# Performance work log

Hardware: AMD Instinct MI355X
Metric: run time of the kernel (lower is better)

## Reference

```python
import jax, jax.numpy as jnp
import numpy as np

B, S, H = 2, 4096, 1024
NKH, NVH, DK, DV = 8, 16, 64, 64
KEY_DIM = NKH * DK
VAL_DIM = NVH * DV
CONV_DIM = 2 * KEY_DIM + VAL_DIM
KSZ = 4
EPS = 1e-6


def setup_inputs() -> dict:
    key = jax.random.key(0)
    ks = jax.random.split(key, 8)
    s = 0.02
    return {
        "hidden_states": jax.random.normal(ks[0], (B, S, H), jnp.float32),
        "W_qkv": jax.random.normal(ks[1], (CONV_DIM, H), jnp.float32) * s,
        "conv_w": jax.random.normal(ks[2], (CONV_DIM, 1, KSZ), jnp.float32) * 0.1,
        "W_z": jax.random.normal(ks[3], (VAL_DIM, H), jnp.float32) * s,
        "W_b": jax.random.normal(ks[4], (NVH, H), jnp.float32) * s,
        "W_a": jax.random.normal(ks[5], (NVH, H), jnp.float32) * s,
        "dt_bias": jnp.ones((NVH,), jnp.float32),
        "A_log": jnp.log(jax.random.uniform(ks[6], (NVH,), jnp.float32, 0.1, 16.0)),
        "norm_weight": jnp.ones((DV,), jnp.float32),
        "W_out": jax.random.normal(ks[7], (H, VAL_DIM), jnp.float32) * s,
    }


def _forward(hidden_states, W_qkv, conv_w, W_z, W_b, W_a, dt_bias, A_log, norm_weight, W_out):
    b, s, _ = hidden_states.shape
    # fused qkv projection -> depthwise causal conv -> silu
    mixed = hidden_states @ W_qkv.T                       # [b,s,conv_dim]
    x = mixed.transpose(0, 2, 1)                          # [b,conv_dim,s]
    y = jax.lax.conv_general_dilated(
        x, conv_w, (1,), [(KSZ - 1, 0)],
        dimension_numbers=("NCH", "OIH", "NCH"),
        feature_group_count=CONV_DIM)                     # causal: left pad k-1
    mixed = jax.nn.silu(y).transpose(0, 2, 1)             # [b,s,conv_dim]

    z = (hidden_states @ W_z.T).reshape(b, s, NVH, DV)
    beta = jax.nn.sigmoid(hidden_states @ W_b.T)          # [b,s,nvh]
    a = hidden_states @ W_a.T
    g = -jnp.exp(A_log) * jax.nn.softplus(a + dt_bias)    # [b,s,nvh]

    q, k, v = jnp.split(mixed, [KEY_DIM, 2 * KEY_DIM], axis=-1)
    q = q.reshape(b, s, NKH, DK)
    k = k.reshape(b, s, NKH, DK)
    v = v.reshape(b, s, NVH, DV)
    rep = NVH // NKH
    if rep > 1:  # GQA: repeat_interleave along head dim
        q = jnp.repeat(q, rep, axis=2)
        k = jnp.repeat(k, rep, axis=2)
    q = q * (DK ** -0.5)

    # gated delta-rule recurrence over time (state: [b,h,dk,dv])
    def step(Sst, inp):
        q_t, k_t, v_t, g_t, b_t = inp                     # [b,h,dk],[b,h,dk],[b,h,dv],[b,h],[b,h]
        Sst = Sst * jnp.exp(g_t)[..., None, None]
        kv = jnp.einsum("bhkv,bhk->bhv", Sst, k_t)
        delta = (v_t - kv) * b_t[..., None]
        Sst = Sst + k_t[..., None] * delta[..., None, :]
        o = jnp.einsum("bhkv,bhk->bhv", Sst, q_t)
        return Sst, o

    S0 = jnp.zeros((b, NVH, DK, DV), jnp.float32)
    xs = (q.transpose(1, 0, 2, 3), k.transpose(1, 0, 2, 3), v.transpose(1, 0, 2, 3),
          g.transpose(1, 0, 2), beta.transpose(1, 0, 2))
    _, o = jax.lax.scan(step, S0, xs)                     # o: [s,b,h,dv]
    o = o.transpose(1, 0, 2, 3)                           # [b,s,h,dv]

    # gated RMSNorm over head_v_dim: x * silu(z), rmsnorm, * weight
    h_ = o * jax.nn.silu(z)
    var = jnp.mean(h_ * h_, axis=-1, keepdims=True)
    h_ = h_ * jax.lax.rsqrt(var + EPS) * norm_weight

    return h_.reshape(b, s, VAL_DIM) @ W_out.T            # [b,s,hidden]


def reference(hidden_states, W_qkv, conv_w, W_z, W_b, W_a, dt_bias, A_log, norm_weight, W_out):
    return _forward(hidden_states, W_qkv, conv_w, W_z, W_b, W_a, dt_bias, A_log, norm_weight, W_out)
```

## Files before the change

kernel.cpp:

```cpp
#include <hip/hip_runtime.h>
#include <hip/hip_bf16.h>
#include <stdint.h>

#define B_    2
#define S_    4096
#define H_    1024
#define NKH_  8
#define NVH_  16
#define DK_   64
#define DV_   64
#define KEYD_ 512
#define CDIM_ 2048
#define VALD_ 1024
#define NCHUNK_ 64
#define CS_   64

using bf16 = __hip_bfloat16;
using bf16x8 = __attribute__((ext_vector_type(8))) short;
using f32x4  = __attribute__((ext_vector_type(4))) float;

__device__ inline float bsh2f(short s) {
  union { ushort u; bf16 h; } c; c.u = (ushort)s; return __bfloat162float(c.h);
}
__device__ inline short f2bsh(float f) {
  union { ushort u; bf16 h; } c; c.h = __float2bfloat16(f); return (short)c.u;
}

__device__ __forceinline__ void gload16(const bf16* g, short* lds) {
  __builtin_amdgcn_global_load_lds(
      (const __attribute__((address_space(1))) void*)g,
      (__attribute__((address_space(3))) void*)lds, 16, 0, 0);
}

__global__ __launch_bounds__(256) void castf2b(const float* __restrict__ x,
                                               bf16* __restrict__ y, long n) {
  const long i = ((long)blockIdx.x * 256 + threadIdx.x) * 4;
  if (i >= n) return;
  float4 v = *(const float4*)(x + i);
  union { ushort4 u; bf16 h[4]; } o;
  o.h[0] = __float2bfloat16(v.x);
  o.h[1] = __float2bfloat16(v.y);
  o.h[2] = __float2bfloat16(v.z);
  o.h[3] = __float2bfloat16(v.w);
  *(ushort4*)(y + i) = o.u;
}

template <typename OT>
__global__ __launch_bounds__(256) void gemm_bt(const bf16* __restrict__ A,
                                               const bf16* __restrict__ Bm,
                                               OT* __restrict__ C,
                                               int M, int N, int K) {
  __shared__ short Asm[128 * 32];
  __shared__ short Bsm[128 * 32];
  const int t = threadIdx.x;
  const int w = t >> 6, l = t & 63;
  const int ntn = N >> 7;
  const int bm = blockIdx.x / ntn, bn = blockIdx.x % ntn;
  const int m0 = bm << 7, n0 = bn << 7;
  const int wm = (w >> 1) << 6, wn = (w & 1) << 6;

  f32x4 acc[4][4] = {};

  const int grow = l >> 2;
  const int gc8 = (l & 3) << 3;
  const bf16* Agl = A + (long)m0 * K + gc8;
  const bf16* Bgl = Bm + (long)n0 * K + gc8;

  const int lm = l & 15;
  const int kk = (l >> 4) << 3;
  const short* ar0 = &Asm[(wm + lm) * 32 + kk];
  const short* br0 = &Bsm[(wn + lm) * 32 + kk];

  for (int k0 = 0; k0 < K; k0 += 32) {
    __syncthreads();
#pragma unroll
    for (int j = 0; j < 2; ++j) {
      const int s = w * 2 + j;
      gload16(Agl + (long)(s * 16 + grow) * K + k0, &Asm[s * 16 * 32]);
      gload16(Bgl + (long)(s * 16 + grow) * K + k0, &Bsm[s * 16 * 32]);
    }
    __syncthreads();
    bf16x8 af[4], bfr[4];
#pragma unroll
    for (int mi = 0; mi < 4; ++mi) af[mi] = *(const bf16x8*)(ar0 + mi * 16 * 32);
#pragma unroll
    for (int ni = 0; ni < 4; ++ni) bfr[ni] = *(const bf16x8*)(br0 + ni * 16 * 32);
#pragma unroll
    for (int mi = 0; mi < 4; ++mi)
#pragma unroll
      for (int ni = 0; ni < 4; ++ni)
        acc[mi][ni] = __builtin_amdgcn_mfma_f32_16x16x32_bf16(af[mi], bfr[ni],
                                                              acc[mi][ni], 0, 0, 0);
  }

  const int r0 = (l >> 4) << 2;
  const int cn = l & 15;
#pragma unroll
  for (int mi = 0; mi < 4; ++mi)
#pragma unroll
    for (int ni = 0; ni < 4; ++ni) {
      long base = (long)(m0 + wm + mi * 16 + r0) * N + (n0 + wn + ni * 16 + cn);
#pragma unroll
      for (int r = 0; r < 4; ++r) {
        if constexpr (sizeof(OT) == 2)
          C[base + (long)r * N] = __float2bfloat16(acc[mi][ni][r]);
        else
          C[base + (long)r * N] = acc[mi][ni][r];
      }
    }
}

__global__ __launch_bounds__(256) void conv3(const bf16* __restrict__ mixed,
                                             const float* __restrict__ cw,
                                             bf16* __restrict__ qkv) {
  const long idx = (long)blockIdx.x * 256 + threadIdx.x;
  const int c0 = (int)(idx & 255) << 3;
  const long row = idx >> 8;
  const int s = (int)(row & (S_ - 1));

  bf16x8 mv[4];
#pragma unroll
  for (int j = 0; j < 4; ++j) {
    if (s - 3 + j >= 0)
      mv[j] = *(const bf16x8*)(mixed + (row + j - 3) * CDIM_ + c0);
    else
      mv[j] = (bf16x8){0, 0, 0, 0, 0, 0, 0, 0};
  }

  const float qs = (c0 < KEYD_) ? 0.125f : 1.f;
  union { ushort4 u4[2]; short h[8]; } o;
#pragma unroll
  for (int e = 0; e < 8; ++e) {
    const float4 w = *(const float4*)(cw + (c0 + e) * 4);
    float acc = 0.f;
    acc = fmaf(w.x, bsh2f(mv[0][e]), acc);
    acc = fmaf(w.y, bsh2f(mv[1][e]), acc);
    acc = fmaf(w.z, bsh2f(mv[2][e]), acc);
    acc = fmaf(w.w, bsh2f(mv[3][e]), acc);
    const float y = qs * (acc / (1.f + __expf(-acc)));
    o.h[e] = f2bsh(y);
  }
  *(bf16x8*)((uint16_t*)qkv + row * CDIM_ + c0) = *(bf16x8*)&o.h[0];
}

__global__ __launch_bounds__(256) void proj_ba2(const float* __restrict__ hs,
                                                const float* __restrict__ Wb,
                                                const float* __restrict__ Wa,
                                                const float* __restrict__ dtb,
                                                const float* __restrict__ Alog,
                                                float* __restrict__ beta,
                                                float* __restrict__ g) {
  __shared__ float4 hrow[8][257];
  const long row0 = (long)blockIdx.x * 8;
  const int tid = threadIdx.x;
  for (int i = tid; i < 2048; i += 256) {
    const int r = i >> 8, c4 = i & 255;
    hrow[r][c4] = *(const float4*)(hs + (row0 + r) * H_ + (long)c4 * 4);
  }
  __syncthreads();
  const int j = tid >> 3, r = tid & 7;
  const float4* Wp = (const float4*)(j < 16 ? Wb + (long)j * H_
                                            : Wa + (long)(j - 16) * H_);
  float4 a4 = {0.f, 0.f, 0.f, 0.f};
#pragma unroll 4
  for (int i = 0; i < 256; ++i) {
    const float4 w = Wp[i];
    const float4 hv = hrow[r][i];
    a4.x = fmaf(w.x, hv.x, a4.x);
    a4.y = fmaf(w.y, hv.y, a4.y);
    a4.z = fmaf(w.z, hv.z, a4.z);
    a4.w = fmaf(w.w, hv.w, a4.w);
  }
  const float acc = (a4.x + a4.y) + (a4.z + a4.w);
  const long row = row0 + r;
  if (j < 16) {
    beta[row * NVH_ + j] = 1.f / (1.f + __expf(-acc));
  } else {
    const int hh = j - 16;
    const float x = acc + dtb[hh];
    const float sp = (x > 20.f) ? x : log1pf(__expf(x));
    g[row * NVH_ + hh] = -__expf(Alog[hh]) * sp;
  }
}

__global__ __launch_bounds__(256) void chunk_pre(const bf16* __restrict__ qkv,
                                                 const float* __restrict__ beta,
                                                 const float* __restrict__ g,
                                                 bf16* __restrict__ Wws,
                                                 bf16* __restrict__ U0ws,
                                                 float* __restrict__ lgws,
                                                 bf16* __restrict__ McT,
                                                 bf16* __restrict__ Bc) {
  __shared__ short Ksm[64][72];
  __shared__ short Vsm[64][72];
  __shared__ float Tsm[64][64];
  __shared__ short KpT[64][72];
  __shared__ float Xl[128][67];
  __shared__ float lgs[64];
  __shared__ float bts[64];
  __shared__ float belg[64];

  short (*XB)[36]   = (short (*)[36]) & Vsm[0][0];
  short (*TloB)[40] = (short (*)[40]) & Ksm[0][0];
  short (*WT)[72]   = (short (*)[72]) & Tsm[0][0];
  short (*U0T)[72]  = Vsm;

  const int blk = blockIdx.x;
  const int hb = blk & 31, c = blk >> 5;
  const long task = (long)hb * 64 + c;
  const int h = hb & 15, b = hb >> 4, kh = h >> 1;
  const long t0 = (long)b * S_ + (long)c * CS_;
  const int tid = threadIdx.x;
  const int wv = tid >> 6, l = tid & 63;
  const int lm = l & 15, lk8 = (l >> 4) << 3;
  const int r0 = (l >> 4) << 2, cn = l & 15;
  const int srow = tid >> 2, scol = (tid & 3) * 16;

  {
    const bf16* kp = qkv + (t0 + srow) * CDIM_ + KEYD_ + kh * 64 + scol;
    const bf16* vp = qkv + (t0 + srow) * CDIM_ + 2 * KEYD_ + h * 64 + scol;
    *(bf16x8*)&Ksm[srow][scol]     = *(const bf16x8*)(kp);
    *(bf16x8*)&Ksm[srow][scol + 8] = *(const bf16x8*)(kp + 8);
    *(bf16x8*)&Vsm[srow][scol]     = *(const bf16x8*)(vp);
    *(bf16x8*)&Vsm[srow][scol + 8] = *(const bf16x8*)(vp + 8);
  }
  if (tid < 64) {
    bts[tid] = beta[(t0 + tid) * NVH_ + h];
    lgs[tid] = g[(t0 + tid) * NVH_ + h];
  }
  __syncthreads();

  if (tid < 64) {
    float x = lgs[tid];
#pragma unroll
    for (int d = 1; d < 64; d <<= 1) {
      const float y = __shfl_up(x, d);
      if (tid >= d) x += y;
    }
    lgs[tid] = x;
    belg[tid] = bts[tid] * __expf(x);
  }
  __syncthreads();

  if (tid < 128) {
    f32x4 acc[2][4] = {};
#pragma unroll
    for (int ks = 0; ks < 2; ++ks) {
      bf16x8 bfr[4];
#pragma unroll
      for (int ni = 0; ni < 4; ++ni)
        bfr[ni] = *(const bf16x8*)&Ksm[ni * 16 + lm][lk8 + ks * 32];
#pragma unroll
      for (int mi = 0; mi < 2; ++mi) {
        bf16x8 afr = *(const bf16x8*)&Ksm[(wv * 2 + mi) * 16 + lm][lk8 + ks * 32];
#pragma unroll
        for (int ni = 0; ni < 4; ++ni)
          acc[mi][ni] = __builtin_amdgcn_mfma_f32_16x16x32_bf16(afr, bfr[ni],
                                                                acc[mi][ni], 0, 0, 0);
      }
    }
#pragma unroll
    for (int mi = 0; mi < 2; ++mi)
#pragma unroll
      for (int ni = 0; ni < 4; ++ni)
#pragma unroll
        for (int r = 0; r < 4; ++r) {
          const int t = (wv * 2 + mi) * 16 + r0 + r;
          const int i = ni * 16 + cn;
          Tsm[t][i] = (i < t) ? bts[t] * __expf(lgs[t] - lgs[i]) * acc[mi][ni][r]
                              : 0.f;
        }
  } else {
    const int idx = tid - 128;
    const int tt = idx >> 1;
    const int o2 = (idx & 1) * 32;
    const float dec = __expf(lgs[63] - lgs[tt]);
#pragma unroll 8
    for (int k = 0; k < 32; ++k)
      KpT[o2 + k][tt] = f2bsh(dec * bsh2f(Ksm[tt][o2 + k]));
  }
  __syncthreads();

  auto solve32 = [&](int base) {
    for (int j = base; j < base + 32; j += 8) {
      float xs[8];
#pragma unroll
      for (int a = 0; a < 8; ++a) xs[a] = Xl[tid][j + a];
#pragma unroll
      for (int a = 1; a < 8; ++a)
#pragma unroll
        for (int bb = 0; bb < a; ++bb)
          xs[a] = fmaf(-Tsm[j + a][j + bb], xs[bb], xs[a]);
#pragma unroll
      for (int a = 1; a < 8; ++a) Xl[tid][j + a] = xs[a];
      const int tend = base + 32;
#pragma unroll 2
      for (int tt = j + 8; tt < tend; ++tt) {
        const float4 ta = *(const float4*)&Tsm[tt][j];
        const float4 tb = *(const float4*)&Tsm[tt][j + 4];
        float v = Xl[tid][tt];
        v = fmaf(-ta.x, xs[0], v); v = fmaf(-ta.y, xs[1], v);
        v = fmaf(-ta.z, xs[2], v); v = fmaf(-ta.w, xs[3], v);
        v = fmaf(-tb.x, xs[4], v); v = fmaf(-tb.y, xs[5], v);
        v = fmaf(-tb.z, xs[6], v); v = fmaf(-tb.w, xs[7], v);
        Xl[tid][tt] = v;
      }
    }
  };

  if (tid < 128) {
    const int colW = tid & 63;
    const bool isW = tid < 64;
#pragma unroll 8
    for (int t = 0; t < CS_; ++t)
      Xl[tid][t] = isW ? belg[t] * bsh2f(Ksm[t][colW])
                       : bts[t] * bsh2f(Vsm[t][colW]);
    solve32(0);
  }
  if (tid < 64) lgws[task * 64 + tid] = lgs[tid];
  __syncthreads();

  {
    const int col = tid & 127, uh = (tid >> 7) * 16;
#pragma unroll
    for (int u = 0; u < 16; ++u)
      XB[col][uh + u] = f2bsh(Xl[col][uh + u]);
  }
  if (tid < 128) {
    const int m = tid >> 2, u0 = (tid & 3) * 8;
#pragma unroll
    for (int u = 0; u < 8; ++u)
      TloB[m][u0 + u] = f2bsh(Tsm[32 + m][u0 + u]);
  }
  __syncthreads();

  {
#pragma unroll
    for (int ni2 = 0; ni2 < 2; ++ni2) {
      const int ni = wv * 2 + ni2;
      bf16x8 bfr = *(const bf16x8*)&XB[ni * 16 + lm][lk8];
#pragma unroll
      for (int mi = 0; mi < 2; ++mi) {
        bf16x8 afr = *(const bf16x8*)&TloB[mi * 16 + lm][lk8];
        f32x4 uacc = {};
        uacc = __builtin_amdgcn_mfma_f32_16x16x32_bf16(afr, bfr, uacc, 0, 0, 0);
#pragma unroll
        for (int r = 0; r < 4; ++r)
          Xl[ni * 16 + cn][32 + mi * 16 + r0 + r] -= uacc[r];
      }
    }
  }
  __syncthreads();

  if (tid < 128) solve32(32);
  __syncthreads();

  if (tid < 128) {
    const int colW = tid & 63;
    const bool isW = tid < 64;
    bf16* dst = (isW ? Wws : U0ws) + task * 4096 + colW;
    short (*XT)[72] = isW ? WT : U0T;
#pragma unroll 4
    for (int t = 0; t < CS_; t += 2) {
      const float v0 = Xl[tid][t], v1 = Xl[tid][t + 1];
      dst[(long)t * 64] = __float2bfloat16(v0);
      dst[(long)(t + 1) * 64] = __float2bfloat16(v1);
      short2 pk; pk.x = f2bsh(v0); pk.y = f2bsh(v1);
      *(short2*)&XT[colW][t] = pk;
    }
  }
  __syncthreads();

  {
    f32x4 macc[4] = {};
#pragma unroll
    for (int ks = 0; ks < 2; ++ks) {
      bf16x8 afr = *(const bf16x8*)&KpT[wv * 16 + lm][lk8 + ks * 32];
#pragma unroll
      for (int ni = 0; ni < 4; ++ni) {
        bf16x8 bfr = *(const bf16x8*)&WT[ni * 16 + lm][lk8 + ks * 32];
        macc[ni] = __builtin_amdgcn_mfma_f32_16x16x32_bf16(afr, bfr, macc[ni], 0, 0, 0);
      }
    }
#pragma unroll
    for (int ni = 0; ni < 4; ++ni)
#pragma unroll
      for (int r = 0; r < 4; ++r)
        McT[task * 4096 + (wv * 16 + r0 + r) * 64 + ni * 16 + cn] =
            __float2bfloat16(-macc[ni][r]);
  }
  {
    f32x4 bacc[4] = {};
#pragma unroll
    for (int ks = 0; ks < 2; ++ks) {
      bf16x8 afr = *(const bf16x8*)&U0T[wv * 16 + lm][lk8 + ks * 32];
#pragma unroll
      for (int ni = 0; ni < 4; ++ni) {
        bf16x8 bfr = *(const bf16x8*)&KpT[ni * 16 + lm][lk8 + ks * 32];
        bacc[ni] = __builtin_amdgcn_mfma_f32_16x16x32_bf16(afr, bfr, bacc[ni], 0, 0, 0);
      }
    }
#pragma unroll
    for (int ni = 0; ni < 4; ++ni)
#pragma unroll
      for (int r = 0; r < 4; ++r)
        Bc[task * 4096 + (wv * 16 + r0 + r) * 64 + ni * 16 + cn] =
            __float2bfloat16(bacc[ni][r]);
  }
}

__global__ __launch_bounds__(256) void chunk_state(const bf16* __restrict__ McT,
                                                   const bf16* __restrict__ Bc,
                                                   const float* __restrict__ lgws,
                                                   bf16* __restrict__ Sb) {
  __shared__ short Msm[3][64][72];
  __shared__ short Bsm[3][64][72];
  __shared__ short Ssm[64][72];
  __shared__ float lgb[3];

  const int hb = blockIdx.x;
  const int tid = threadIdx.x, wv = tid >> 6, l = tid & 63;
  const int lm = l & 15, lk8 = (l >> 4) << 3;
  const int r0 = (l >> 4) << 2, cn = l & 15;
  const int srow = tid >> 2, scol = (tid & 3) * 16;

  for (int i = tid; i < 64 * 72; i += 256) ((short*)Ssm)[i] = 0;
  f32x4 Sreg[4] = {};

  auto stage = [&](int cc, int bu) {
    const long tt = (long)hb * 64 + cc;
    const bf16* mp = McT + tt * 4096 + srow * 64 + scol;
    const bf16* bp = Bc + tt * 4096 + srow * 64 + scol;
    *(bf16x8*)&Msm[bu][srow][scol]     = *(const bf16x8*)(mp);
    *(bf16x8*)&Msm[bu][srow][scol + 8] = *(const bf16x8*)(mp + 8);
    *(bf16x8*)&Bsm[bu][srow][scol]     = *(const bf16x8*)(bp);
    *(bf16x8*)&Bsm[bu][srow][scol + 8] = *(const bf16x8*)(bp + 8);
    if (tid == 0) lgb[bu] = lgws[tt * 64 + 63];
  };
  stage(0, 0);
  stage(1, 1);

  for (int c = 0; c < NCHUNK_; ++c) {
    __syncthreads();
    if (c + 2 < NCHUNK_) stage(c + 2, (c + 2) % 3);
    const int bu = c % 3;

    {
      bf16* sp = Sb + ((long)hb * 64 + c) * 4096;
#pragma unroll
      for (int ni = 0; ni < 4; ++ni)
#pragma unroll
        for (int r = 0; r < 4; ++r)
          sp[(wv * 16 + r0 + r) * 64 + ni * 16 + cn] = __float2bfloat16(Sreg[ni][r]);
    }

    bf16x8 sfr0 = *(const bf16x8*)&Ssm[wv * 16 + lm][lk8];
    bf16x8 sfr1 = *(const bf16x8*)&Ssm[wv * 16 + lm][lk8 + 32];
    f32x4 kacc[4] = {};
#pragma unroll
    for (int ni = 0; ni < 4; ++ni) {
      bf16x8 b0 = *(const bf16x8*)&Msm[bu][ni * 16 + lm][lk8];
      kacc[ni] = __builtin_amdgcn_mfma_f32_16x16x32_bf16(sfr0, b0, kacc[ni], 0, 0, 0);
      bf16x8 b1 = *(const bf16x8*)&Msm[bu][ni * 16 + lm][lk8 + 32];
      kacc[ni] = __builtin_amdgcn_mfma_f32_16x16x32_bf16(sfr1, b1, kacc[ni], 0, 0, 0);
    }
    const float eend = __expf(lgb[bu]);
#pragma unroll
    for (int ni = 0; ni < 4; ++ni)
#pragma unroll
      for (int r = 0; r < 4; ++r) {
        const float bv = bsh2f(Bsm[bu][wv * 16 + r0 + r][ni * 16 + cn]);
        Sreg[ni][r] = eend * Sreg[ni][r] + kacc[ni][r] + bv;
        Ssm[wv * 16 + r0 + r][ni * 16 + cn] = f2bsh(Sreg[ni][r]);
      }
  }
}

__global__ __launch_bounds__(256) void chunk_out(const bf16* __restrict__ qkv,
                                                 const bf16* __restrict__ Wws,
                                                 const bf16* __restrict__ U0ws,
                                                 const float* __restrict__ lgws,
                                                 const bf16* __restrict__ Sb,
                                                 float* __restrict__ o) {
  __shared__ short Qsm[64][72];
  __shared__ short Ksm[64][72];
  __shared__ short Wsm[64][72];
  __shared__ short Usm[64][72];
  __shared__ short Amm[64][72];
  __shared__ short Dsm[64][72];
  __shared__ float lgs[64];

  const int blk = blockIdx.x;
  const int hb = blk & 31, c = blk >> 5;
  const long task = (long)hb * 64 + c;
  const int h = hb & 15, b = hb >> 4, kh = h >> 1;
  const long sb = (long)b * S_ + (long)c * CS_;
  const int tid = threadIdx.x, wv = tid >> 6, l = tid & 63;
  const int lm = l & 15, lk8 = (l >> 4) << 3;
  const int r0 = (l >> 4) << 2, cn = l & 15;
  const int srow = tid >> 2, scol = (tid & 3) * 16;

  const bf16* sp = Sb + task * 4096 + (wv * 16 + lm) * 64 + lk8;
  bf16x8 sfr0 = *(const bf16x8*)(sp);
  bf16x8 sfr1 = *(const bf16x8*)(sp + 32);

  {
    const bf16* qp = qkv + (sb + srow) * CDIM_ + kh * 64 + scol;
    const bf16* kp = qkv + (sb + srow) * CDIM_ + KEYD_ + kh * 64 + scol;
    const bf16* wp = Wws + task * 4096 + srow * 64 + scol;
    const bf16* up = U0ws + task * 4096 + srow * 64 + scol;
    *(bf16x8*)&Qsm[srow][scol]     = *(const bf16x8*)(qp);
    *(bf16x8*)&Qsm[srow][scol + 8] = *(const bf16x8*)(qp + 8);
    *(bf16x8*)&Ksm[srow][scol]     = *(const bf16x8*)(kp);
    *(bf16x8*)&Ksm[srow][scol + 8] = *(const bf16x8*)(kp + 8);
    *(bf16x8*)&Wsm[srow][scol]     = *(const bf16x8*)(wp);
    *(bf16x8*)&Wsm[srow][scol + 8] = *(const bf16x8*)(wp + 8);
    *(bf16x8*)&Usm[srow][scol]     = *(const bf16x8*)(up);
    *(bf16x8*)&Usm[srow][scol + 8] = *(const bf16x8*)(up + 8);
    if (tid < 64) lgs[tid] = lgws[task * 64 + tid];
  }
  __syncthreads();

  {
    f32x4 aacc[4] = {};
#pragma unroll
    for (int ks = 0; ks < 2; ++ks) {
      bf16x8 qa = *(const bf16x8*)&Qsm[wv * 16 + lm][lk8 + ks * 32];
#pragma unroll
      for (int ni = 0; ni < 4; ++ni) {
        bf16x8 kb = *(const bf16x8*)&Ksm[ni * 16 + lm][lk8 + ks * 32];
        aacc[ni] = __builtin_amdgcn_mfma_f32_16x16x32_bf16(qa, kb, aacc[ni], 0, 0, 0);
      }
    }
#pragma unroll
    for (int ni = 0; ni < 4; ++ni)
#pragma unroll
      for (int r = 0; r < 4; ++r) {
        const int t = wv * 16 + r0 + r, i = ni * 16 + cn;
        Amm[t][i] = f2bsh((i <= t) ? aacc[ni][r] * __expf(lgs[t] - lgs[i]) : 0.f);
      }
  }
  __syncthreads();

  {
    const float sc = __expf(lgs[srow]);
#pragma unroll
    for (int j = 0; j < 16; ++j)
      Qsm[srow][scol + j] = f2bsh(sc * bsh2f(Qsm[srow][scol + j]));
  }
  __syncthreads();

  {
    f32x4 dacc[4] = {};
#pragma unroll
    for (int ni = 0; ni < 4; ++ni) {
      bf16x8 w0 = *(const bf16x8*)&Wsm[ni * 16 + lm][lk8];
      dacc[ni] = __builtin_amdgcn_mfma_f32_16x16x32_bf16(sfr0, w0, dacc[ni], 0, 0, 0);
      bf16x8 w1 = *(const bf16x8*)&Wsm[ni * 16 + lm][lk8 + 32];
      dacc[ni] = __builtin_amdgcn_mfma_f32_16x16x32_bf16(sfr1, w1, dacc[ni], 0, 0, 0);
    }
#pragma unroll
    for (int ni = 0; ni < 4; ++ni)
#pragma unroll
      for (int r = 0; r < 4; ++r) {
        const int t = ni * 16 + cn, v = r0 + r;
        Dsm[wv * 16 + v][t] = f2bsh(bsh2f(Usm[t][wv * 16 + v]) - dacc[ni][r]);
      }
  }
  bf16x8 dfr0 = *(const bf16x8*)&Dsm[wv * 16 + lm][lk8];
  bf16x8 dfr1 = *(const bf16x8*)&Dsm[wv * 16 + lm][lk8 + 32];

  {
    f32x4 oacc[4] = {};
#pragma unroll
    for (int mi = 0; mi < 4; ++mi) {
      bf16x8 q0 = *(const bf16x8*)&Qsm[mi * 16 + lm][lk8];
      oacc[mi] = __builtin_amdgcn_mfma_f32_16x16x32_bf16(q0, sfr0, oacc[mi], 0, 0, 0);
      bf16x8 q1 = *(const bf16x8*)&Qsm[mi * 16 + lm][lk8 + 32];
      oacc[mi] = __builtin_amdgcn_mfma_f32_16x16x32_bf16(q1, sfr1, oacc[mi], 0, 0, 0);
    }
#pragma unroll
    for (int mi = 0; mi < 4; ++mi) {
      bf16x8 a0 = *(const bf16x8*)&Amm[mi * 16 + lm][lk8];
      oacc[mi] = __builtin_amdgcn_mfma_f32_16x16x32_bf16(a0, dfr0, oacc[mi], 0, 0, 0);
      bf16x8 a1 = *(const bf16x8*)&Amm[mi * 16 + lm][lk8 + 32];
      oacc[mi] = __builtin_amdgcn_mfma_f32_16x16x32_bf16(a1, dfr1, oacc[mi], 0, 0, 0);
    }
#pragma unroll
    for (int mi = 0; mi < 4; ++mi)
#pragma unroll
      for (int r = 0; r < 4; ++r) {
        const int t = mi * 16 + r0 + r;
        o[(sb + t) * VALD_ + h * 64 + wv * 16 + cn] = oacc[mi][r];
      }
  }
}

__global__ __launch_bounds__(256) void gnorm3(const float* __restrict__ o,
                                              const float* __restrict__ z,
                                              const float* __restrict__ nw,
                                              bf16* __restrict__ hn) {
  const long idx = (long)blockIdx.x * 256 + threadIdx.x;
  const float* op = o + idx * 64;
  const float* zp = z + idx * 64;
  float4 hv[16];
  float ss = 0.f;
#pragma unroll
  for (int i = 0; i < 16; ++i) {
    const float4 ov = *(const float4*)(op + i * 4);
    const float4 zv = *(const float4*)(zp + i * 4);
    float4 h;
    h.x = ov.x * (zv.x / (1.f + __expf(-zv.x)));
    h.y = ov.y * (zv.y / (1.f + __expf(-zv.y)));
    h.z = ov.z * (zv.z / (1.f + __expf(-zv.z)));
    h.w = ov.w * (zv.w / (1.f + __expf(-zv.w)));
    hv[i] = h;
    ss = fmaf(h.x, h.x, ss); ss = fmaf(h.y, h.y, ss);
    ss = fmaf(h.z, h.z, ss); ss = fmaf(h.w, h.w, ss);
  }
  const float r = rsqrtf(ss * (1.f / 64.f) + 1e-6f);
#pragma unroll
  for (int i = 0; i < 16; i += 2) {
    const float4 w0 = *(const float4*)(nw + i * 4);
    const float4 w1 = *(const float4*)(nw + i * 4 + 4);
    bf16x8 pk;
    pk[0] = f2bsh(hv[i].x * r * w0.x);     pk[1] = f2bsh(hv[i].y * r * w0.y);
    pk[2] = f2bsh(hv[i].z * r * w0.z);     pk[3] = f2bsh(hv[i].w * r * w0.w);
    pk[4] = f2bsh(hv[i + 1].x * r * w1.x); pk[5] = f2bsh(hv[i + 1].y * r * w1.y);
    pk[6] = f2bsh(hv[i + 1].z * r * w1.z); pk[7] = f2bsh(hv[i + 1].w * r * w1.w);
    *(bf16x8*)((uint16_t*)hn + idx * 64 + i * 4) = pk;
  }
}

extern "C" void kernel_launch(void* const* d_in, const int* in_sizes, int n_in,
                              void* d_out, int out_size, void* d_ws, size_t ws_size,
                              hipStream_t stream) {
  float* out = (float*)d_out;
  const int M = B_ * S_;

  int ih, iqkv, icw, iz, ib, ia, idtb, ialog, inw, iout;
  if (n_in >= 10 && in_sizes[0] == 8388608) {
    ih = 0; iqkv = 1; icw = 2; iz = 3; ib = 4; ia = 5;
    idtb = 6; ialog = 7; inw = 8; iout = 9;
  } else {
    ih = iqkv = icw = iz = ib = ia = idtb = ialog = inw = iout = -1;
    for (int i = 0; i < n_in; ++i) {
      switch (in_sizes[i]) {
        case 8388608: ih = i; break;
        case 2097152: iqkv = i; break;
        case 8192:    icw = i; break;
        case 64:      inw = i; break;
        case 1048576: if (iz < 0) iz = i; else iout = i; break;
        case 16384:   if (ib < 0) ib = i; else ia = i; break;
        case 16:      if (idtb < 0) idtb = i; else ialog = i; break;
        default: break;
      }
    }
  }
  const float* hs   = (const float*)d_in[ih];
  const float* Wqkv = (const float*)d_in[iqkv];
  const float* cw   = (const float*)d_in[icw];
  const float* Wz   = (const float*)d_in[iz];
  const float* Wb   = (const float*)d_in[ib];
  const float* Wa   = (const float*)d_in[ia];
  const float* dtb  = (const float*)d_in[idtb];
  const float* Alog = (const float*)d_in[ialog];
  const float* nwv  = (const float*)d_in[inw];
  const float* Wout = (const float*)d_in[iout];

  char* p = (char*)d_ws;
  bf16*  mixed = (bf16*)p;
  float* of    = (float*)p;
  bf16*  McTw  = (bf16*)p;
  bf16*  Bcw   = (bf16*)(p + (size_t)2048 * 4096 * 2);
  p += (size_t)M * CDIM_ * 2;
  bf16*  hs_b  = (bf16*)p;
  bf16*  qkvb  = (bf16*)p;
  bf16*  hn    = (bf16*)p; p += (size_t)M * CDIM_ * 2;
  bf16*  Wqkv_b= (bf16*)p; p += (size_t)CDIM_ * H_ * 2;
  bf16*  Wz_b  = (bf16*)p; p += (size_t)H_ * H_ * 2;
  bf16*  Wout_b= (bf16*)p; p += (size_t)H_ * H_ * 2;
  float* betaf = (float*)p; p += (size_t)M * NVH_ * 4;
  float* gf    = (float*)p; p += (size_t)M * NVH_ * 4;
  bf16*  Wws   = (bf16*)p; p += (size_t)2048 * 4096 * 2;
  bf16*  U0ws  = (bf16*)p; p += (size_t)2048 * 4096 * 2;
  float* lgws  = (float*)p; p += (size_t)2048 * 64 * 4;
  bf16*  Sbw   = (bf16*)p; p += (size_t)2048 * 4096 * 2;
  float* zb    = out;

  {
    long n;
    n = (long)M * H_;     castf2b<<<(int)(n / 4 / 256), 256, 0, stream>>>(hs,   hs_b,   n);
    n = (long)CDIM_ * H_; castf2b<<<(int)(n / 4 / 256), 256, 0, stream>>>(Wqkv, Wqkv_b, n);
    n = (long)H_ * H_;    castf2b<<<(int)(n / 4 / 256), 256, 0, stream>>>(Wz,   Wz_b,   n);
    n = (long)H_ * H_;    castf2b<<<(int)(n / 4 / 256), 256, 0, stream>>>(Wout, Wout_b, n);
  }
  gemm_bt<bf16><<<(M / 128) * (CDIM_ / 128), 256, 0, stream>>>(hs_b, Wqkv_b, mixed, M, CDIM_, H_);
  gemm_bt<float><<<(M / 128) * (H_ / 128), 256, 0, stream>>>(hs_b, Wz_b, zb, M, H_, H_);
  proj_ba2<<<M / 8, 256, 0, stream>>>(hs, Wb, Wa, dtb, Alog, betaf, gf);
  conv3<<<(int)(((long)M * CDIM_) / 8 / 256), 256, 0, stream>>>(mixed, cw, qkvb);
  chunk_pre<<<2048, 256, 0, stream>>>(qkvb, betaf, gf, Wws, U0ws, lgws, McTw, Bcw);
  chunk_state<<<32, 256, 0, stream>>>(McTw, Bcw, lgws, Sbw);
  chunk_out<<<2048, 256, 0, stream>>>(qkvb, Wws, U0ws, lgws, Sbw, of);
  gnorm3<<<(M * NVH_) / 256, 256, 0, stream>>>(of, zb, nwv, hn);
  gemm_bt<float><<<(M / 128) * (H_ / 128), 256, 0, stream>>>(hn, Wout_b, out, M, H_, H_);
}
```

Before: 502.3 us.

## Batch chunk_state into groups of four chunks with register-prefetched double buffering

The serial inter-chunk state kernel now stages four chunks at a time. It prefetches the next group from global memory into registers while the current group computes, and writes them to a double-buffered shared-memory array. Barriers drop from one per chunk to one per group of four. This relies on each wave reading back only its own rows of the shared state tile. The aim is to cut barrier and load-latency stalls on the sequential critical path, in exchange for higher register and LDS use.

```diff
diff --git a/kernel.cpp b/kernel.cpp
--- a/kernel.cpp
+++ b/kernel.cpp
@@ -413,10 +413,10 @@
                                                    const bf16* __restrict__ Bc,
                                                    const float* __restrict__ lgws,
                                                    bf16* __restrict__ Sb) {
-  __shared__ short Msm[3][64][72];
-  __shared__ short Bsm[3][64][72];
+  __shared__ short Msm[2][4][64][72];
+  __shared__ short Bsm[2][4][64][72];
   __shared__ short Ssm[64][72];
-  __shared__ float lgb[3];
+  __shared__ float lgsm[2][4];
 
   const int hb = blockIdx.x;
   const int tid = threadIdx.x, wv = tid >> 6, l = tid & 63;
@@ -427,52 +427,82 @@
   for (int i = tid; i < 64 * 72; i += 256) ((short*)Ssm)[i] = 0;
   f32x4 Sreg[4] = {};
 
-  auto stage = [&](int cc, int bu) {
-    const long tt = (long)hb * 64 + cc;
-    const bf16* mp = McT + tt * 4096 + srow * 64 + scol;
-    const bf16* bp = Bc + tt * 4096 + srow * 64 + scol;
-    *(bf16x8*)&Msm[bu][srow][scol]     = *(const bf16x8*)(mp);
-    *(bf16x8*)&Msm[bu][srow][scol + 8] = *(const bf16x8*)(mp + 8);
-    *(bf16x8*)&Bsm[bu][srow][scol]     = *(const bf16x8*)(bp);
-    *(bf16x8*)&Bsm[bu][srow][scol + 8] = *(const bf16x8*)(bp + 8);
-    if (tid == 0) lgb[bu] = lgws[tt * 64 + 63];
+  bf16x8 mr0[4], mr1[4], br0[4], br1[4];
+  float lgn0, lgn1, lgn2, lgn3;
+
+  auto gload = [&](int g) {
+#pragma unroll
+    for (int cc = 0; cc < 4; ++cc) {
+      const long tt = (long)hb * 64 + g * 4 + cc;
+      const bf16* mp = McT + tt * 4096 + srow * 64 + scol;
+      const bf16* bp = Bc + tt * 4096 + srow * 64 + scol;
+      mr0[cc] = *(const bf16x8*)(mp);
+      mr1[cc] = *(const bf16x8*)(mp + 8);
+      br0[cc] = *(const bf16x8*)(bp);
+      br1[cc] = *(const bf16x8*)(bp + 8);
+    }
+    const long tb = (long)hb * 64 + g * 4;
+    lgn0 = lgws[(tb + 0) * 64 + 63];
+    lgn1 = lgws[(tb + 1) * 64 + 63];
+    lgn2 = lgws[(tb + 2) * 64 + 63];
+    lgn3 = lgws[(tb + 3) * 64 + 63];
   };
-  stage(0, 0);
-  stage(1, 1);
-
-  for (int c = 0; c < NCHUNK_; ++c) {
+  auto lwrite = [&](int g) {
+    const int bu = g & 1;
+#pragma unroll
+    for (int cc = 0; cc < 4; ++cc) {
+      *(bf16x8*)&Msm[bu][cc][srow][scol]     = mr0[cc];
+      *(bf16x8*)&Msm[bu][cc][srow][scol + 8] = mr1[cc];
+      *(bf16x8*)&Bsm[bu][cc][srow][scol]     = br0[cc];
+      *(bf16x8*)&Bsm[bu][cc][srow][scol + 8] = br1[cc];
+    }
+    if (tid == 0) {
+      lgsm[bu][0] = lgn0; lgsm[bu][1] = lgn1;
+      lgsm[bu][2] = lgn2; lgsm[bu][3] = lgn3;
+    }
+  };
+
+  gload(0);
+  lwrite(0);
+  gload(1);
+  __syncthreads();
+
+  for (int g = 0; g < 16; ++g) {
+    const int bu = g & 1;
+    if (g + 1 < 16) lwrite(g + 1);
+    if (g + 2 < 16) gload(g + 2);
+#pragma unroll
+    for (int cc = 0; cc < 4; ++cc) {
+      const int c = g * 4 + cc;
+      {
+        bf16* sp = Sb + ((long)hb * 64 + c) * 4096;
+#pragma unroll
+        for (int ni = 0; ni < 4; ++ni)
+#pragma unroll
+          for (int r = 0; r < 4; ++r)
+            sp[(wv * 16 + r0 + r) * 64 + ni * 16 + cn] = __float2bfloat16(Sreg[ni][r]);
+      }
+      bf16x8 sfr0 = *(const bf16x8*)&Ssm[wv * 16 + lm][lk8];
+      bf16x8 sfr1 = *(const bf16x8*)&Ssm[wv * 16 + lm][lk8 + 32];
+      f32x4 kacc[4] = {};
+#pragma unroll
+      for (int ni = 0; ni < 4; ++ni) {
+        bf16x8 b0 = *(const bf16x8*)&Msm[bu][cc][ni * 16 + lm][lk8];
+        kacc[ni] = __builtin_amdgcn_mfma_f32_16x16x32_bf16(sfr0, b0, kacc[ni], 0, 0, 0);
+        bf16x8 b1 = *(const bf16x8*)&Msm[bu][cc][ni * 16 + lm][lk8 + 32];
+        kacc[ni] = __builtin_amdgcn_mfma_f32_16x16x32_bf16(sfr1, b1, kacc[ni], 0, 0, 0);
+      }
+      const float eend = __expf(lgsm[bu][cc]);
+#pragma unroll
+      for (int ni = 0; ni < 4; ++ni)
+#pragma unroll
+        for (int r = 0; r < 4; ++r) {
+          const float bv = bsh2f(Bsm[bu][cc][wv * 16 + r0 + r][ni * 16 + cn]);
+          Sreg[ni][r] = eend * Sreg[ni][r] + kacc[ni][r] + bv;
+          Ssm[wv * 16 + r0 + r][ni * 16 + cn] = f2bsh(Sreg[ni][r]);
+        }
+    }
     __syncthreads();
-    if (c + 2 < NCHUNK_) stage(c + 2, (c + 2) % 3);
-    const int bu = c % 3;
-
-    {
-      bf16* sp = Sb + ((long)hb * 64 + c) * 4096;
-#pragma unroll
-      for (int ni = 0; ni < 4; ++ni)
-#pragma unroll
-        for (int r = 0; r < 4; ++r)
-          sp[(wv * 16 + r0 + r) * 64 + ni * 16 + cn] = __float2bfloat16(Sreg[ni][r]);
-    }
-
-    bf16x8 sfr0 = *(const bf16x8*)&Ssm[wv * 16 + lm][lk8];
-    bf16x8 sfr1 = *(const bf16x8*)&Ssm[wv * 16 + lm][lk8 + 32];
-    f32x4 kacc[4] = {};
-#pragma unroll
-    for (int ni = 0; ni < 4; ++ni) {
-      bf16x8 b0 = *(const bf16x8*)&Msm[bu][ni * 16 + lm][lk8];
-      kacc[ni] = __builtin_amdgcn_mfma_f32_16x16x32_bf16(sfr0, b0, kacc[ni], 0, 0, 0);
-      bf16x8 b1 = *(const bf16x8*)&Msm[bu][ni * 16 + lm][lk8 + 32];
-      kacc[ni] = __builtin_amdgcn_mfma_f32_16x16x32_bf16(sfr1, b1, kacc[ni], 0, 0, 0);
-    }
-    const float eend = __expf(lgb[bu]);
-#pragma unroll
-    for (int ni = 0; ni < 4; ++ni)
-#pragma unroll
-      for (int r = 0; r < 4; ++r) {
-        const float bv = bsh2f(Bsm[bu][wv * 16 + r0 + r][ni * 16 + cn]);
-        Sreg[ni][r] = eend * Sreg[ni][r] + kacc[ni][r] + bv;
-        Ssm[wv * 16 + r0 + r][ni * 16 + cn] = f2bsh(Sreg[ni][r]);
-      }
   }
 }
 
```

Result: faster. 477.8 us (-4.9%).
